# Kernel optimization log

Measured on AMD Instinct MI355X. Metric: run time of the kernel, lower is better.

## Reference

```python
import jax, jax.numpy as jnp
import numpy as np
import math

B, S, K, D, H, LH, W, L = 8, 2048, 128, 512, 8, 4, 128, 4
DH = D // H           # 64, head dim
NW = S // W           # 16 windows
NUM_STEPS = 1000
RESCALE = 4000.0


def setup_inputs() -> dict:
    key = jax.random.key(0)
    ks = iter(jax.random.split(key, 48))
    def rn(shape, s=0.02):
        return jax.random.normal(next(ks), shape, dtype=jnp.float32) * s
    return {
        "x": jax.random.normal(next(ks), (B, S, K), dtype=jnp.float32),
        "t": jax.random.randint(next(ks), (B,), 0, NUM_STEPS, dtype=jnp.int32),
        "token_w": rn((K, D)), "token_b": jnp.zeros((D,), jnp.float32),
        "ax1": rn((NW, D), 1.0), "ax2": rn((W, D), 1.0),
        "time_w1": rn((D, 4 * D)), "time_b1": jnp.zeros((4 * D,), jnp.float32),
        "time_w2": rn((4 * D, D)), "time_b2": jnp.zeros((D,), jnp.float32),
        "ln1_g": jnp.ones((L, D), jnp.float32), "ln1_b": jnp.zeros((L, D), jnp.float32),
        "wq": rn((L, D, D)), "wk": rn((L, D, D)), "wv": rn((L, D, D)),
        "wo": rn((L, D, D)), "wo_b": jnp.zeros((L, D), jnp.float32),
        "ln2_g": jnp.ones((L, D), jnp.float32), "ln2_b": jnp.zeros((L, D), jnp.float32),
        "ff_w1": rn((L, D, 4 * D)), "ff_b1": jnp.zeros((L, 4 * D), jnp.float32),
        "ff_w2": rn((L, 4 * D, D)), "ff_b2": jnp.zeros((L, D), jnp.float32),
        "norm_g": jnp.ones((D,), jnp.float32), "norm_b": jnp.zeros((D,), jnp.float32),
        "out_w": rn((D, K)), "out_b": jnp.zeros((K,), jnp.float32),
        "alpha": jax.random.normal(next(ks), (1,), dtype=jnp.float32),
    }


def _layernorm(x, g, b, eps=1e-5):
    mu = x.mean(-1, keepdims=True)
    var = ((x - mu) ** 2).mean(-1, keepdims=True)
    return (x - mu) * jax.lax.rsqrt(var + eps) * g + b


def _mish(x):
    return x * jnp.tanh(jax.nn.softplus(x))


def _sinusoidal(t):
    # SinusoidalPosEmb(dim=D, num_steps=NUM_STEPS, rescale_steps=4000)
    tt = t.astype(jnp.float32) / NUM_STEPS * RESCALE
    half = D // 2
    freqs = jnp.exp(jnp.arange(half, dtype=jnp.float32) * (-math.log(10000.0) / (half - 1)))
    e = tt[:, None] * freqs[None, :]
    return jnp.concatenate([jnp.sin(e), jnp.cos(e)], axis=-1)  # (B, D)


def _linear_attn(q, k, v):
    # non-causal kernelized linear attention; q,k,v: (B, h, S, dh)
    scale = DH ** -0.25
    q = jax.nn.softmax(q * scale, axis=-1)   # softmax over feature dim
    k = jax.nn.softmax(k * scale, axis=-2)   # softmax over sequence dim
    ctx = jnp.einsum('bhnd,bhne->bhde', k, v)
    return jnp.einsum('bhnd,bhde->bhne', q, ctx)


def _local_attn(q, k, v):
    # windowed softmax attention, window W, look_backward=1, look_forward=1
    b, h = q.shape[0], q.shape[1]
    qw = q.reshape(b, h, NW, W, DH) * (DH ** -0.5)
    def look_around(x):
        xw = x.reshape(b, h, NW, W, DH)
        xp = jnp.pad(xw, ((0, 0), (0, 0), (1, 1), (0, 0), (0, 0)))
        # keys of windows [i-1, i, i+1] -> (b, h, NW, 3W, dh)
        return jnp.concatenate([xp[:, :, :-2], xp[:, :, 1:-1], xp[:, :, 2:]], axis=3)
    kw, vw = look_around(k), look_around(v)
    win = jnp.arange(NW)[:, None] + (jnp.arange(3 * W) // W)[None, :] - 1  # (NW, 3W)
    valid = (win >= 0) & (win < NW)
    dots = jnp.einsum('bhnwd,bhnkd->bhnwk', qw, kw)
    mask_value = -jnp.finfo(dots.dtype).max
    dots = jnp.where(valid[None, None, :, None, :], dots, mask_value)
    attn = jax.nn.softmax(dots, axis=-1)
    out = jnp.einsum('bhnwk,bhnkd->bhnwd', attn, vw)
    return out.reshape(b, h, S, DH)


def reference(x, t, token_w, token_b, ax1, ax2, time_w1, time_b1, time_w2, time_b2,
              ln1_g, ln1_b, wq, wk, wv, wo, wo_b, ln2_g, ln2_b,
              ff_w1, ff_b1, ff_w2, ff_b2, norm_g, norm_b, out_w, out_b, alpha):
    te = _sinusoidal(t)
    te = _mish(te @ time_w1 + time_b1) @ time_w2 + time_b2          # (B, D)
    h = x @ token_w + token_b                                        # token embedding
    pos = (ax1[:, None, :] + ax2[None, :, :]).reshape(S, D)          # axial pos emb (summed)
    h = h + pos[None] + te[:, None, :]
    for l in range(L):
        n = _layernorm(h, ln1_g[l], ln1_b[l])
        def split_heads(y):
            return y.reshape(B, S, H, DH).transpose(0, 2, 1, 3)
        q = split_heads(n @ wq[l]); k = split_heads(n @ wk[l]); v = split_heads(n @ wv[l])
        lo = _local_attn(q[:, :LH], k[:, :LH], v[:, :LH])            # local heads first
        gl = _linear_attn(q[:, LH:], k[:, LH:], v[:, LH:])           # global linear-attn heads
        a = jnp.concatenate([lo, gl], axis=1).transpose(0, 2, 1, 3).reshape(B, S, D)
        h = h + a @ wo[l] + wo_b[l]
        n = _layernorm(h, ln2_g[l], ln2_b[l])
        h = h + jax.nn.gelu(n @ ff_w1[l] + ff_b1[l], approximate=False) @ ff_w2[l] + ff_b2[l]
    out = _layernorm(h, norm_g, norm_b) @ out_w + out_b              # (B, S, K)
    return alpha * out.transpose(0, 2, 1)                            # permute + Rezero -> (B, K, S)
```

## Files before the change

kernel.cpp:

```cpp
#include <hip/hip_runtime.h>

typedef __bf16 bf16;
typedef float f32x4 __attribute__((ext_vector_type(4)));
typedef __bf16 b8v __attribute__((ext_vector_type(8)));
typedef __bf16 b4v __attribute__((ext_vector_type(4)));

#define S_LEN 2048
#define DMODEL 512
#define KDIM 128
#define NWIN 16
#define WIN 128
#define QKVS 1536

__device__ inline f32x4 mfma16(b8v a, b8v b, f32x4 c) {
  return __builtin_amdgcn_mfma_f32_16x16x32_bf16(a, b, c, 0, 0, 0);
}

__device__ inline void gload16(const bf16* g, bf16* l) {
  __builtin_amdgcn_global_load_lds(
      (const __attribute__((address_space(1))) void*)g,
      (__attribute__((address_space(3))) void*)l, 16, 0, 0);
}

template<int N>
__device__ inline void waitvm() { asm volatile("s_waitcnt vmcnt(%0)" :: "n"(N) : "memory"); }
__device__ inline void barrier_raw() { asm volatile("s_barrier" ::: "memory"); }


__global__ __launch_bounds__(256) void conv_kernel(const float* __restrict__ in, bf16* __restrict__ out, int n) {
  int i4 = (blockIdx.x * 256 + threadIdx.x) * 4;
  if (i4 < n) {
    float4 v = *(const float4*)(in + i4);
    b4v o; o[0] = (bf16)v.x; o[1] = (bf16)v.y; o[2] = (bf16)v.z; o[3] = (bf16)v.w;
    *(b4v*)(out + i4) = o;
  }
}

__global__ __launch_bounds__(256) void convT_kernel(const float* __restrict__ W, bf16* __restrict__ WT,
                                                    int Kd, int N, size_t in_ls, size_t out_ls) {
  __shared__ float tile[32][33];
  int k0 = blockIdx.x * 32, n0 = blockIdx.y * 32;
  const float* Wl = W + (size_t)blockIdx.z * in_ls;
  bf16* WTl = WT + (size_t)blockIdx.z * out_ls;
  int tx = threadIdx.x & 31, ty = threadIdx.x >> 5;
  #pragma unroll
  for (int i = 0; i < 4; i++)
    tile[ty + i*8][tx] = Wl[(size_t)(k0 + ty + i*8) * N + n0 + tx];
  __syncthreads();
  #pragma unroll
  for (int i = 0; i < 4; i++)
    WTl[(size_t)(n0 + ty + i*8) * Kd + k0 + tx] = (bf16)tile[tx][ty + i*8];
}


__global__ __launch_bounds__(256) void time1_kernel(const int* __restrict__ t,
    const float* __restrict__ w1, const float* __restrict__ b1, float* __restrict__ te1) {
  __shared__ float te[512];
  __shared__ float red[4][64];
  int b = blockIdx.x >> 5;
  int c0 = (blockIdx.x & 31) * 64;
  int tid = threadIdx.x;
  float tt = (float)t[b] * 4.0f;
  {
    float fr = expf((float)tid * (-9.210340371976184f / 255.0f));
    float e = tt * fr;
    te[tid] = sinf(e);
    te[tid + 256] = cosf(e);
  }
  __syncthreads();
  int lane = tid & 63, wv = tid >> 6;
  float acc = 0.f;
  const float* wcol = w1 + (size_t)(wv * 128) * 2048 + c0 + lane;
  for (int dd = 0; dd < 128; dd++) acc = fmaf(te[wv * 128 + dd], wcol[(size_t)dd * 2048], acc);
  red[wv][lane] = acc;
  __syncthreads();
  if (tid < 64) {
    float a = red[0][tid] + red[1][tid] + red[2][tid] + red[3][tid] + b1[c0 + tid];
    float sp = (a > 20.f) ? a : log1pf(expf(a));
    te1[b * 2048 + c0 + tid] = a * tanhf(sp);
  }
}

__global__ __launch_bounds__(256) void time2_kernel(const float* __restrict__ te1,
    const float* __restrict__ w2, const float* __restrict__ b2, float* __restrict__ te2) {
  __shared__ float hb[2048];
  __shared__ float red[4][64];
  int b = blockIdx.x >> 3;
  int c0 = (blockIdx.x & 7) * 64;
  int tid = threadIdx.x;
  for (int i = tid; i < 2048; i += 256) hb[i] = te1[b * 2048 + i];
  __syncthreads();
  int lane = tid & 63, wv = tid >> 6;
  float acc = 0.f;
  const float* wcol = w2 + (size_t)(wv * 512) * 512 + c0 + lane;
  for (int dd = 0; dd < 512; dd++) acc = fmaf(hb[wv * 512 + dd], wcol[(size_t)dd * 512], acc);
  red[wv][lane] = acc;
  __syncthreads();
  if (tid < 64)
    te2[b * 512 + c0 + tid] = red[0][tid] + red[1][tid] + red[2][tid] + red[3][tid] + b2[c0 + tid];
}


__global__ __launch_bounds__(256) void ln_kernel(const float* __restrict__ hsrc,
    const float* __restrict__ gg, const float* __restrict__ bb, bf16* __restrict__ out) {
  int row = blockIdx.x * 4 + (threadIdx.x >> 6);
  int lane = threadIdx.x & 63;
  const float* hr = hsrc + (size_t)row * 512 + lane * 8;
  float4 v0 = *(const float4*)hr;
  float4 v1 = *(const float4*)(hr + 4);
  float xv[8] = {v0.x, v0.y, v0.z, v0.w, v1.x, v1.y, v1.z, v1.w};
  float s = 0.f;
  #pragma unroll
  for (int j = 0; j < 8; j++) s += xv[j];
  #pragma unroll
  for (int off = 1; off < 64; off <<= 1) s += __shfl_xor(s, off);
  float mu = s * (1.f / 512.f);
  float vs = 0.f;
  #pragma unroll
  for (int j = 0; j < 8; j++) { float dd = xv[j] - mu; vs += dd * dd; }
  #pragma unroll
  for (int off = 1; off < 64; off <<= 1) vs += __shfl_xor(vs, off);
  float rstd = 1.f / sqrtf(vs * (1.f / 512.f) + 1e-5f);
  int dbase = lane * 8;
  bf16* orow = out + (size_t)row * 512 + dbase;
  #pragma unroll
  for (int j = 0; j < 8; j++)
    orow[j] = (bf16)((xv[j] - mu) * rstd * gg[dbase + j] + bb[dbase + j]);
}

template<int EPI, int BM, int BN>
__global__ __launch_bounds__(512, 2) void gemm2_kernel(
    const bf16* __restrict__ A, const bf16* __restrict__ BT,
    const float* __restrict__ bias, float* __restrict__ Cf, bf16* __restrict__ Cb,
    int N, int Kd, int nbx) {
  constexpr int LA = BM / 128;
  constexpr int LB = BN / 128;
  constexpr int LPI = LA + LB;
  constexpr int EA = BM * 32;
  constexpr int EB = BN * 32;
  constexpr int ER = EA + EB;
  constexpr int MF = BM / 32;
  constexpr int NF = BN / 64;
  __shared__ bf16 lds[ER * 3];
  int tid = threadIdx.x;
  int lane = tid & 63, wid = tid >> 6;
  int g = lane >> 4, lr = lane & 15;
  int wm = wid >> 2, wn = wid & 3;
  int p = blockIdx.x;
  int cpx = (int)gridDim.x >> 3;
  int vid = (p & 7) * cpx + (p >> 3);
  int m0 = (vid / nbx) * BM;
  int n0 = (vid % nbx) * BN;
  f32x4 acc[MF][NF] = {};
  int rl = tid >> 2;
  int csw = ((tid & 3) ^ ((rl >> 1) & 3)) * 8;
  const bf16* pa = A + (size_t)(m0 + rl) * Kd + csw;
  const bf16* pb = BT + (size_t)(n0 + rl) * Kd + csw;
  int NT = Kd >> 5;
  auto stage = [&](int t, int buf) {
    int k0 = t << 5;
    bf16* base = lds + buf * ER + (wid << 9);
    #pragma unroll
    for (int rr = 0; rr < LA; rr++)
      gload16(pa + (size_t)(rr * 128) * Kd + k0, base + rr * 4096);
    #pragma unroll
    for (int rr = 0; rr < LB; rr++)
      gload16(pb + (size_t)(rr * 128) * Kd + k0, base + EA + rr * 4096);
  };
  stage(0, 0);
  stage(1, 1);
  waitvm<LPI>();
  barrier_raw();
  for (int t = 0; t < NT; ++t) {
    if (t + 2 < NT) stage(t + 2, (t + 2) % 3);
    const bf16* ba = lds + (t % 3) * ER;
    const bf16* bb = ba + EA;
    b8v af[MF], bfr[NF];
    #pragma unroll
    for (int i = 0; i < MF; i++) {
      int ra = wm * (BM / 2) + i * 16 + lr;
      af[i] = *(const b8v*)(ba + ra * 32 + ((g * 8) ^ (((ra >> 1) & 3) << 3)));
    }
    #pragma unroll
    for (int j = 0; j < NF; j++) {
      int rb = wn * (BN / 4) + j * 16 + lr;
      bfr[j] = *(const b8v*)(bb + rb * 32 + ((g * 8) ^ (((rb >> 1) & 3) << 3)));
    }
    __builtin_amdgcn_s_setprio(1);
    #pragma unroll
    for (int i = 0; i < MF; i++)
      #pragma unroll
      for (int j = 0; j < NF; j++)
        acc[i][j] = mfma16(af[i], bfr[j], acc[i][j]);
    __builtin_amdgcn_s_setprio(0);
    if (t + 1 < NT) {
      if (t + 2 < NT) waitvm<LPI>();
      else            waitvm<0>();
      barrier_raw();
    }
  }
  #pragma unroll
  for (int i = 0; i < MF; i++) {
    #pragma unroll
    for (int j = 0; j < NF; j++) {
      int col = n0 + wn * (BN / 4) + j * 16 + lr;
      float bv = (EPI != 0) ? bias[col] : 0.0f;
      #pragma unroll
      for (int r = 0; r < 4; r++) {
        int row = m0 + wm * (BM / 2) + i * 16 + g * 4 + r;
        float v = acc[i][j][r] + bv;
        if (EPI == 0) {
          Cb[(size_t)row * N + col] = (bf16)v;
        } else if (EPI == 2) {
          Cf[(size_t)row * N + col] += v;
        } else if (EPI == 3) {
          float ge = 0.5f * v * (1.0f + erff(v * 0.70710678118654752f));
          Cb[(size_t)row * N + col] = (bf16)ge;
        }
      }
    }
  }
}

template<int EPI>
__global__ __launch_bounds__(256) void gemm_kernel(
    const bf16* __restrict__ A, const bf16* __restrict__ BT,
    const float* __restrict__ bias, float* __restrict__ Cf, bf16* __restrict__ Cb,
    int N, int Kd, int nbx,
    const float* __restrict__ q1, const float* __restrict__ q2, const float* __restrict__ q3,
    const float* __restrict__ alphap) {
  __shared__ bf16 As[2][4096];
  __shared__ bf16 Bs[2][4096];
  int tid = threadIdx.x;
  int lane = tid & 63, wid = tid >> 6;
  int g = lane >> 4, lr = lane & 15;
  int wm = wid >> 1, wn = wid & 1;
  int p = blockIdx.x;
  int cpx = (int)gridDim.x >> 3;
  int vid = (p & 7) * cpx + (p >> 3);
  int m0 = (vid / nbx) * 128;
  int n0 = (vid % nbx) * 128;
  f32x4 acc[4][4] = {};
  int srow = wid * 16 + (lane >> 2);
  int scol = (lane & 3) * 8;
  const bf16* pa = A + (size_t)(m0 + srow) * Kd + scol;
  const bf16* pb = BT + (size_t)(n0 + srow) * Kd + scol;
  const size_t rstep = (size_t)64 * Kd;
  int nt = Kd >> 5;
  auto stage = [&](int buf, int k0) {
    bf16* lA = &As[buf][wid * 512];
    bf16* lB = &Bs[buf][wid * 512];
    gload16(pa + k0, lA);
    gload16(pa + rstep + k0, lA + 2048);
    gload16(pb + k0, lB);
    gload16(pb + rstep + k0, lB + 2048);
  };
  stage(0, 0);
  __syncthreads();
  int cur = 0;
  for (int t = 0; t < nt; ++t) {
    if (t + 1 < nt) stage(cur ^ 1, (t + 1) * 32);
    b8v af[4], bfv[4];
    #pragma unroll
    for (int i = 0; i < 4; i++) af[i]  = *(const b8v*)&As[cur][(wm * 64 + i * 16 + lr) * 32 + g * 8];
    #pragma unroll
    for (int i = 0; i < 4; i++) bfv[i] = *(const b8v*)&Bs[cur][(wn * 64 + i * 16 + lr) * 32 + g * 8];
    #pragma unroll
    for (int mf = 0; mf < 4; mf++)
      #pragma unroll
      for (int nf = 0; nf < 4; nf++)
        acc[mf][nf] = mfma16(af[mf], bfv[nf], acc[mf][nf]);
    __syncthreads();
    cur ^= 1;
  }
  if constexpr (EPI == 4) {
    __shared__ float Ts[32][130];
    float alp = alphap[0];
    int b_ = m0 >> 11, sb = m0 & 2047;
    #pragma unroll
    for (int cg = 0; cg < 4; cg++) {
      __syncthreads();
      if (wn == (cg >> 1)) {
        #pragma unroll
        for (int nfi = 0; nfi < 2; nfi++) {
          int nf = (cg & 1) * 2 + nfi;
          int cl = nfi * 16 + lr;
          float bv = bias[cg * 32 + cl];
          #pragma unroll
          for (int mf = 0; mf < 4; mf++)
            #pragma unroll
            for (int r = 0; r < 4; r++)
              Ts[cl][wm * 64 + mf * 16 + g * 4 + r] = alp * (acc[mf][nf][r] + bv);
        }
      }
      __syncthreads();
      int cl = tid >> 3, soff = (tid & 7) * 16;
      int col = cg * 32 + cl;
      float* dst = Cf + (size_t)b_ * (KDIM * S_LEN) + (size_t)col * S_LEN + sb + soff;
      #pragma unroll
      for (int q4 = 0; q4 < 4; q4++) {
        float4 v = {Ts[cl][soff + q4*4], Ts[cl][soff + q4*4 + 1], Ts[cl][soff + q4*4 + 2], Ts[cl][soff + q4*4 + 3]};
        *(float4*)(dst + q4 * 4) = v;
      }
    }
    return;
  }
  #pragma unroll
  for (int mf = 0; mf < 4; mf++) {
    #pragma unroll
    for (int nf = 0; nf < 4; nf++) {
      int col = n0 + wn * 64 + nf * 16 + lr;
      float bv = bias[col];
      #pragma unroll
      for (int r = 0; r < 4; r++) {
        int row = m0 + wm * 64 + mf * 16 + g * 4 + r;
        float v = acc[mf][nf][r] + bv;
        if (EPI == 5) {
          int b_ = row >> 11, s_ = row & 2047;
          float pv = q1[(s_ >> 7) * 512 + col] + q2[(s_ & 127) * 512 + col] + q3[b_ * 512 + col];
          Cf[(size_t)row * N + col] = v + pv;
        }
      }
    }
  }
}

__global__ __launch_bounds__(256) void locattn_kernel(
    const bf16* __restrict__ qkv, bf16* __restrict__ ab) {
  __shared__ bf16 Ks[128][72];
  __shared__ bf16 Vt[64][136];
  __shared__ bf16 Ps[4][32][136];
  int w = blockIdx.x;
  int b = blockIdx.y >> 2, hh = blockIdx.y & 3;
  int tid = threadIdx.x, wid = tid >> 6, lane = tid & 63;
  int g = lane >> 4, lr = lane & 15;
  const size_t rowb = (size_t)b * S_LEN * QKVS;
  int qrow0 = w * WIN + wid * 32;
  b8v qf[2][2];
  #pragma unroll
  for (int mf = 0; mf < 2; mf++)
    #pragma unroll
    for (int kf = 0; kf < 2; kf++)
      qf[mf][kf] = *(const b8v*)(qkv + rowb + (size_t)(qrow0 + mf * 16 + lr) * QKVS + hh * 64 + kf * 32 + g * 8);
  float mrun[2][4], lrun[2][4];
  f32x4 oacc[2][4] = {};
  #pragma unroll
  for (int mf = 0; mf < 2; mf++)
    #pragma unroll
    for (int r = 0; r < 4; r++) { mrun[mf][r] = -3e38f; lrun[mf][r] = 0.f; }
  for (int c = 0; c < 3; c++) {
    int wc = w - 1 + c;
    if (wc < 0 || wc >= NWIN) continue;
    __syncthreads();
    {
      int row = tid >> 1, f0 = (tid & 1) * 32;
      const bf16* kp = qkv + rowb + (size_t)(wc * WIN + row) * QKVS + 512 + hh * 64 + f0;
      #pragma unroll
      for (int i = 0; i < 4; i++)
        *(b8v*)&Ks[row][f0 + i * 8] = *(const b8v*)(kp + i * 8);
      const bf16* vp = qkv + rowb + (size_t)(wc * WIN + row) * QKVS + 1024 + hh * 64 + f0;
      #pragma unroll
      for (int i = 0; i < 4; i++) {
        b8v vv = *(const b8v*)(vp + i * 8);
        #pragma unroll
        for (int j = 0; j < 8; j++) Vt[f0 + i * 8 + j][row] = vv[j];
      }
    }
    __syncthreads();
    f32x4 sc[2][8] = {};
    #pragma unroll
    for (int nf = 0; nf < 8; nf++) {
      #pragma unroll
      for (int kf = 0; kf < 2; kf++) {
        b8v kfr = *(const b8v*)&Ks[nf * 16 + lr][kf * 32 + g * 8];
        sc[0][nf] = mfma16(qf[0][kf], kfr, sc[0][nf]);
        sc[1][nf] = mfma16(qf[1][kf], kfr, sc[1][nf]);
      }
    }
    #pragma unroll
    for (int mf = 0; mf < 2; mf++) {
      #pragma unroll
      for (int r = 0; r < 4; r++) {
        float cm = -3e38f;
        #pragma unroll
        for (int nf = 0; nf < 8; nf++) { sc[mf][nf][r] *= 0.125f; cm = fmaxf(cm, sc[mf][nf][r]); }
        cm = fmaxf(cm, __shfl_xor(cm, 1));
        cm = fmaxf(cm, __shfl_xor(cm, 2));
        cm = fmaxf(cm, __shfl_xor(cm, 4));
        cm = fmaxf(cm, __shfl_xor(cm, 8));
        float mnew = fmaxf(mrun[mf][r], cm);
        float corr = __expf(mrun[mf][r] - mnew);
        float rs = 0.f;
        #pragma unroll
        for (int nf = 0; nf < 8; nf++) { float p = __expf(sc[mf][nf][r] - mnew); sc[mf][nf][r] = p; rs += p; }
        rs += __shfl_xor(rs, 1); rs += __shfl_xor(rs, 2);
        rs += __shfl_xor(rs, 4); rs += __shfl_xor(rs, 8);
        lrun[mf][r] = lrun[mf][r] * corr + rs;
        mrun[mf][r] = mnew;
        #pragma unroll
        for (int vf = 0; vf < 4; vf++) oacc[mf][vf][r] *= corr;
      }
    }
    #pragma unroll
    for (int mf = 0; mf < 2; mf++)
      #pragma unroll
      for (int nf = 0; nf < 8; nf++)
        #pragma unroll
        for (int r = 0; r < 4; r++)
          Ps[wid][mf * 16 + g * 4 + r][nf * 16 + lr] = (bf16)sc[mf][nf][r];
    #pragma unroll
    for (int kf2 = 0; kf2 < 4; kf2++) {
      b8v pa0 = *(const b8v*)&Ps[wid][lr][kf2 * 32 + g * 8];
      b8v pa1 = *(const b8v*)&Ps[wid][16 + lr][kf2 * 32 + g * 8];
      #pragma unroll
      for (int vf = 0; vf < 4; vf++) {
        b8v vv = *(const b8v*)&Vt[vf * 16 + lr][kf2 * 32 + g * 8];
        oacc[0][vf] = mfma16(pa0, vv, oacc[0][vf]);
        oacc[1][vf] = mfma16(pa1, vv, oacc[1][vf]);
      }
    }
  }
  #pragma unroll
  for (int mf = 0; mf < 2; mf++) {
    #pragma unroll
    for (int r = 0; r < 4; r++) {
      float inv = 1.0f / lrun[mf][r];
      int row = qrow0 + mf * 16 + g * 4 + r;
      #pragma unroll
      for (int vf = 0; vf < 4; vf++)
        ab[(size_t)b * S_LEN * DMODEL + (size_t)row * DMODEL + hh * 64 + vf * 16 + lr] = (bf16)(oacc[mf][vf][r] * inv);
    }
  }
}


__global__ __launch_bounds__(256) void la2_kernel(const bf16* __restrict__ qkv,
    float* __restrict__ part, float* __restrict__ psum) {
  int ch = blockIdx.x, bh = blockIdx.y;
  int b = bh >> 2, hh = bh & 3;
  __shared__ float ke[128][65];
  __shared__ float vsh[128][65];
  __shared__ float red[4][64];
  int tid = threadIdx.x;
  const float scale = 0.35355339059327373f;
  const size_t base = ((size_t)b * S_LEN + (size_t)ch * 128) * QKVS;
  const bf16* kp = qkv + base + 768 + hh * 64;
  const bf16* vp = qkv + base + 1280 + hh * 64;
  for (int i = tid; i < 1024; i += 256) {
    int s = i >> 3, d0 = (i & 7) * 8;
    b8v kv = *(const b8v*)(kp + (size_t)s * QKVS + d0);
    b8v vv = *(const b8v*)(vp + (size_t)s * QKVS + d0);
    #pragma unroll
    for (int j = 0; j < 8; j++) {
      ke[s][d0 + j] = __expf((float)kv[j] * scale);
      vsh[s][d0 + j] = (float)vv[j];
    }
  }
  __syncthreads();
  int d = tid & 63, sg = tid >> 6;
  float ps = 0.f;
  for (int s = sg * 32; s < sg * 32 + 32; s++) ps += ke[s][d];
  red[sg][d] = ps;
  int e = tid & 63, dg = tid >> 6;
  float accv[16] = {};
  for (int s = 0; s < 128; s++) {
    float vv2 = vsh[s][e];
    #pragma unroll
    for (int i = 0; i < 16; i++) accv[i] = fmaf(ke[s][dg * 16 + i], vv2, accv[i]);
  }
  __syncthreads();
  float* pp = part + ((size_t)ch * 32 + bh) * 4096 + (size_t)dg * 16 * 64 + e;
  #pragma unroll
  for (int i = 0; i < 16; i++) pp[i * 64] = accv[i];
  if (tid < 64)
    psum[((size_t)ch * 32 + bh) * 64 + tid] = red[0][tid] + red[1][tid] + red[2][tid] + red[3][tid];
}

__global__ __launch_bounds__(256) void la2b_kernel(const float* __restrict__ part,
    const float* __restrict__ psum, float* __restrict__ ctx) {
  int idx = blockIdx.x * 256 + threadIdx.x;
  int bh = idx >> 12;
  int d = (idx >> 6) & 63;
  float s = 0.f, cs = 0.f;
  for (int c = 0; c < 16; c++) {
    s += part[(size_t)c * 131072 + idx];
    cs += psum[(size_t)(c * 32 + bh) * 64 + d];
  }
  ctx[idx] = s / cs;
}

__global__ __launch_bounds__(256) void la3_kernel(const bf16* __restrict__ qkv,
    const float* __restrict__ ctx, bf16* __restrict__ ab) {
  int ch = blockIdx.x, bh = blockIdx.y;
  int b = bh >> 2, hh = bh & 3;
  __shared__ float cs[64][65];
  int tid = threadIdx.x;
  for (int i = tid; i < 4096; i += 256) cs[i >> 6][i & 63] = ctx[(size_t)bh * 4096 + i];
  __syncthreads();
  int s = ch * 128 + (tid >> 1);
  int e0 = (tid & 1) * 32;
  const float scale = 0.35355339059327373f;
  const bf16* qr = qkv + ((size_t)b * S_LEN + s) * QKVS + 256 + hh * 64;
  float qv[64];
  float mx = -3e38f;
  #pragma unroll
  for (int i = 0; i < 8; i++) {
    b8v qq = *(const b8v*)(qr + i * 8);
    #pragma unroll
    for (int j = 0; j < 8; j++) { qv[i * 8 + j] = (float)qq[j] * scale; mx = fmaxf(mx, qv[i * 8 + j]); }
  }
  float sum = 0.f;
  #pragma unroll
  for (int dd = 0; dd < 64; dd++) { qv[dd] = __expf(qv[dd] - mx); sum += qv[dd]; }
  float inv = 1.f / sum;
  float o[32] = {};
  #pragma unroll
  for (int dd = 0; dd < 64; dd++) {
    float qq = qv[dd] * inv;
    #pragma unroll
    for (int j = 0; j < 32; j++) o[j] = fmaf(qq, cs[dd][e0 + j], o[j]);
  }
  bf16* op = ab + ((size_t)b * S_LEN + s) * DMODEL + 256 + hh * 64 + e0;
  #pragma unroll
  for (int j = 0; j < 32; j++) op[j] = (bf16)o[j];
}


extern "C" void kernel_launch(void* const* d_in, const int* in_sizes, int n_in,
                              void* d_out, int out_size, void* d_ws, size_t ws_size,
                              hipStream_t stream) {
  (void)in_sizes; (void)n_in; (void)out_size; (void)ws_size;
  const float* x_f     = (const float*)d_in[0];
  const int*   t_i     = (const int*)  d_in[1];
  const float* token_w = (const float*)d_in[2];
  const float* token_b = (const float*)d_in[3];
  const float* ax1     = (const float*)d_in[4];
  const float* ax2     = (const float*)d_in[5];
  const float* time_w1 = (const float*)d_in[6];
  const float* time_b1 = (const float*)d_in[7];
  const float* time_w2 = (const float*)d_in[8];
  const float* time_b2 = (const float*)d_in[9];
  const float* ln1_g   = (const float*)d_in[10];
  const float* ln1_b   = (const float*)d_in[11];
  const float* wq      = (const float*)d_in[12];
  const float* wk      = (const float*)d_in[13];
  const float* wv      = (const float*)d_in[14];
  const float* wo      = (const float*)d_in[15];
  const float* wo_b    = (const float*)d_in[16];
  const float* ln2_g   = (const float*)d_in[17];
  const float* ln2_b   = (const float*)d_in[18];
  const float* ff_w1   = (const float*)d_in[19];
  const float* ff_b1   = (const float*)d_in[20];
  const float* ff_w2   = (const float*)d_in[21];
  const float* ff_b2   = (const float*)d_in[22];
  const float* norm_g  = (const float*)d_in[23];
  const float* norm_b  = (const float*)d_in[24];
  const float* out_w   = (const float*)d_in[25];
  const float* out_b   = (const float*)d_in[26];
  const float* alpha   = (const float*)d_in[27];

  char* ws = (char*)d_ws;
  float* h      = (float*)(ws + 0);
  float* te1    = (float*)(ws + 33554432);
  float* te2    = (float*)(ws + 33619968);
  float* psum   = (float*)(ws + 33636352);
  float* ctx    = (float*)(ws + 33767424);
  float* part   = (float*)(ws + 34291712);
  bf16* nbuf    = (bf16*)(ws + 42680320);
  bf16* qkvb    = (bf16*)(ws + 59457536);
  bf16* abuf    = (bf16*)(ws + 109789184);
  bf16* gbuf    = qkvb;
  bf16* xw      = (bf16*)(ws + 126566400);
  bf16* token_wT= (bf16*)(ws + 130760704);
  bf16* wqkvT   = (bf16*)(ws + 130891776);
  bf16* woT     = (bf16*)(ws + 137183232);
  bf16* ff1T    = (bf16*)(ws + 139280384);
  bf16* ff2T    = (bf16*)(ws + 147668992);
  bf16* outwT   = (bf16*)(ws + 156057600);

  conv_kernel<<<2048, 256, 0, stream>>>(x_f, xw, 2097152);
  convT_kernel<<<dim3(4, 16, 1),  256, 0, stream>>>(token_w, token_wT, 128, 512, 65536, 65536);
  convT_kernel<<<dim3(16, 16, 4), 256, 0, stream>>>(wq, wqkvT,           512, 512, 262144, 786432);
  convT_kernel<<<dim3(16, 16, 4), 256, 0, stream>>>(wk, wqkvT + 262144,  512, 512, 262144, 786432);
  convT_kernel<<<dim3(16, 16, 4), 256, 0, stream>>>(wv, wqkvT + 524288,  512, 512, 262144, 786432);
  convT_kernel<<<dim3(16, 16, 4), 256, 0, stream>>>(wo, woT, 512, 512, 262144, 262144);
  convT_kernel<<<dim3(16, 64, 4), 256, 0, stream>>>(ff_w1, ff1T, 512, 2048, 1048576, 1048576);
  convT_kernel<<<dim3(64, 16, 4), 256, 0, stream>>>(ff_w2, ff2T, 2048, 512, 1048576, 1048576);
  convT_kernel<<<dim3(16, 4, 1),  256, 0, stream>>>(out_w, outwT, 512, 128, 65536, 65536);

  time1_kernel<<<256, 256, 0, stream>>>(t_i, time_w1, time_b1, te1);
  time2_kernel<<<64, 256, 0, stream>>>(te1, time_w2, time_b2, te2);

  gemm_kernel<5><<<512, 256, 0, stream>>>(xw, token_wT, token_b, h, nullptr, 512, 128, 4, ax1, ax2, te2, nullptr);

  for (int l = 0; l < 4; l++) {
    ln_kernel<<<4096, 256, 0, stream>>>(h, ln1_g + l * 512, ln1_b + l * 512, nbuf);
    gemm2_kernel<0, 128, 256><<<768, 512, 0, stream>>>(nbuf, wqkvT + (size_t)l * 786432, nullptr, nullptr, qkvb, 1536, 512, 6);
    locattn_kernel<<<dim3(16, 32), 256, 0, stream>>>(qkvb, abuf);
    la2_kernel<<<dim3(16, 32), 256, 0, stream>>>(qkvb, part, psum);
    la2b_kernel<<<512, 256, 0, stream>>>(part, psum, ctx);
    la3_kernel<<<dim3(16, 32), 256, 0, stream>>>(qkvb, ctx, abuf);
    gemm2_kernel<2, 128, 256><<<256, 512, 0, stream>>>(abuf, woT + (size_t)l * 262144, wo_b + l * 512, h, nullptr, 512, 512, 2);
    ln_kernel<<<4096, 256, 0, stream>>>(h, ln2_g + l * 512, ln2_b + l * 512, nbuf);
    gemm2_kernel<3, 256, 256><<<512, 512, 0, stream>>>(nbuf, ff1T + (size_t)l * 1048576, ff_b1 + l * 2048, nullptr, gbuf, 2048, 512, 8);
    gemm2_kernel<2, 128, 256><<<256, 512, 0, stream>>>(gbuf, ff2T + (size_t)l * 1048576, ff_b2 + l * 512, h, nullptr, 512, 2048, 2);
  }

  ln_kernel<<<4096, 256, 0, stream>>>(h, norm_g, norm_b, nbuf);
  gemm_kernel<4><<<128, 256, 0, stream>>>(nbuf, outwT, out_b, (float*)d_out, nullptr, 128, 512, 1, nullptr, nullptr, nullptr, alpha);
}
```

Baseline: 1.109 ms.

## Interleave B-fragment LDS loads with MFMAs and use tanh-approx GELU

Restructures the GEMM main loop so the wait and barrier come at the top of each k-step and the next prefetch is issued after the barrier. B fragments are then loaded from LDS one column-group ahead, with explicit lgkmcnt waits and sched barriers, so LDS reads overlap the MFMA issue. Separately, the exact erf-based GELU in the FF1 epilogue is replaced by the tanh approximation written as a sigmoid with __expf. That is cheaper but deviates from the reference's exact GELU.

```diff
diff --git a/kernel.cpp b/kernel.cpp
--- a/kernel.cpp
+++ b/kernel.cpp
@@ -24,6 +24,8 @@
 
 template<int N>
 __device__ inline void waitvm() { asm volatile("s_waitcnt vmcnt(%0)" :: "n"(N) : "memory"); }
+template<int N>
+__device__ inline void waitlgkm() { asm volatile("s_waitcnt lgkmcnt(%0)" :: "n"(N) : "memory"); }
 __device__ inline void barrier_raw() { asm volatile("s_barrier" ::: "memory"); }
 
 
@@ -129,7 +131,7 @@
 }
 
 template<int EPI, int BM, int BN>
-__global__ __launch_bounds__(512, 2) void gemm2_kernel(
+__global__ __launch_bounds__(512, 2) void gemm3_kernel(
     const bf16* __restrict__ A, const bf16* __restrict__ BT,
     const float* __restrict__ bias, float* __restrict__ Cf, bf16* __restrict__ Cb,
     int N, int Kd, int nbx) {
@@ -169,12 +171,13 @@
   };
   stage(0, 0);
   stage(1, 1);
-  waitvm<LPI>();
-  barrier_raw();
-  for (int t = 0; t < NT; ++t) {
-    if (t + 2 < NT) stage(t + 2, (t + 2) % 3);
-    const bf16* ba = lds + (t % 3) * ER;
+  for (int kt = 0; kt < NT; ++kt) {
+    if (kt + 1 < NT) waitvm<LPI>();
+    else             waitvm<0>();
+    barrier_raw();
+    const bf16* ba = lds + (kt % 3) * ER;
     const bf16* bb = ba + EA;
+    if (kt + 2 < NT) stage(kt + 2, (kt + 2) % 3);
     b8v af[MF], bfr[NF];
     #pragma unroll
     for (int i = 0; i < MF; i++) {
@@ -182,21 +185,30 @@
       af[i] = *(const b8v*)(ba + ra * 32 + ((g * 8) ^ (((ra >> 1) & 3) << 3)));
     }
     #pragma unroll
-    for (int j = 0; j < NF; j++) {
-      int rb = wn * (BN / 4) + j * 16 + lr;
-      bfr[j] = *(const b8v*)(bb + rb * 32 + ((g * 8) ^ (((rb >> 1) & 3) << 3)));
-    }
+    for (int j0 = 0; j0 < 2; j0++) {
+      int rb = wn * (BN / 4) + j0 * 16 + lr;
+      bfr[j0] = *(const b8v*)(bb + rb * 32 + ((g * 8) ^ (((rb >> 1) & 3) << 3)));
+    }
+    waitlgkm<0>();
+    __builtin_amdgcn_sched_barrier(0);
     __builtin_amdgcn_s_setprio(1);
     #pragma unroll
-    for (int i = 0; i < MF; i++)
-      #pragma unroll
-      for (int j = 0; j < NF; j++)
-        acc[i][j] = mfma16(af[i], bfr[j], acc[i][j]);
+    for (int i = 0; i < MF; i++) acc[i][0] = mfma16(af[i], bfr[0], acc[i][0]);
     __builtin_amdgcn_s_setprio(0);
-    if (t + 1 < NT) {
-      if (t + 2 < NT) waitvm<LPI>();
-      else            waitvm<0>();
-      barrier_raw();
+    #pragma unroll
+    for (int j = 1; j < NF; j++) {
+      if (j + 1 < NF) {
+        int rb = wn * (BN / 4) + (j + 1) * 16 + lr;
+        bfr[j + 1] = *(const b8v*)(bb + rb * 32 + ((g * 8) ^ (((rb >> 1) & 3) << 3)));
+        waitlgkm<1>();
+      } else {
+        waitlgkm<0>();
+      }
+      __builtin_amdgcn_sched_barrier(0);
+      __builtin_amdgcn_s_setprio(1);
+      #pragma unroll
+      for (int i = 0; i < MF; i++) acc[i][j] = mfma16(af[i], bfr[j], acc[i][j]);
+      __builtin_amdgcn_s_setprio(0);
     }
   }
   #pragma unroll
@@ -214,7 +226,8 @@
         } else if (EPI == 2) {
           Cf[(size_t)row * N + col] += v;
         } else if (EPI == 3) {
-          float ge = 0.5f * v * (1.0f + erff(v * 0.70710678118654752f));
+          float u = 1.5957691216057308f * (v + 0.044715f * v * v * v);
+          float ge = v / (1.0f + __expf(-u));
           Cb[(size_t)row * N + col] = (bf16)ge;
         }
       }
@@ -595,15 +608,15 @@
 
   for (int l = 0; l < 4; l++) {
     ln_kernel<<<4096, 256, 0, stream>>>(h, ln1_g + l * 512, ln1_b + l * 512, nbuf);
-    gemm2_kernel<0, 128, 256><<<768, 512, 0, stream>>>(nbuf, wqkvT + (size_t)l * 786432, nullptr, nullptr, qkvb, 1536, 512, 6);
+    gemm3_kernel<0, 128, 256><<<768, 512, 0, stream>>>(nbuf, wqkvT + (size_t)l * 786432, nullptr, nullptr, qkvb, 1536, 512, 6);
     locattn_kernel<<<dim3(16, 32), 256, 0, stream>>>(qkvb, abuf);
     la2_kernel<<<dim3(16, 32), 256, 0, stream>>>(qkvb, part, psum);
     la2b_kernel<<<512, 256, 0, stream>>>(part, psum, ctx);
     la3_kernel<<<dim3(16, 32), 256, 0, stream>>>(qkvb, ctx, abuf);
-    gemm2_kernel<2, 128, 256><<<256, 512, 0, stream>>>(abuf, woT + (size_t)l * 262144, wo_b + l * 512, h, nullptr, 512, 512, 2);
+    gemm3_kernel<2, 128, 256><<<256, 512, 0, stream>>>(abuf, woT + (size_t)l * 262144, wo_b + l * 512, h, nullptr, 512, 512, 2);
     ln_kernel<<<4096, 256, 0, stream>>>(h, ln2_g + l * 512, ln2_b + l * 512, nbuf);
-    gemm2_kernel<3, 256, 256><<<512, 512, 0, stream>>>(nbuf, ff1T + (size_t)l * 1048576, ff_b1 + l * 2048, nullptr, gbuf, 2048, 512, 8);
-    gemm2_kernel<2, 128, 256><<<256, 512, 0, stream>>>(gbuf, ff2T + (size_t)l * 1048576, ff_b2 + l * 512, h, nullptr, 512, 2048, 2);
+    gemm3_kernel<3, 256, 256><<<512, 512, 0, stream>>>(nbuf, ff1T + (size_t)l * 1048576, ff_b1 + l * 2048, nullptr, gbuf, 2048, 512, 8);
+    gemm3_kernel<2, 128, 256><<<256, 512, 0, stream>>>(gbuf, ff2T + (size_t)l * 1048576, ff_b2 + l * 512, h, nullptr, 512, 2048, 2);
   }
 
   ln_kernel<<<4096, 256, 0, stream>>>(h, norm_g, norm_b, nbuf);
```

After: 1.092 ms. About the same (-1.5%).

## Restructure GEMM to 256-row tiles with interleaved LDS loads and tanh GELU

Applied to the files above, without the earlier changes.

Replaces the GEMM kernel with a variant that always uses 256-row A tiles. For the QKV, WO and FF2 GEMMs the tile is now 256x128 instead of 128x256. The K-loop moves the wait/barrier to the top and issues the next stage after it, then splits the A-fragment LDS reads into phases interleaved with MFMA groups using sched_barrier. The FF1 epilogue swaps exact erf GELU for the tanh approximation written as a sigmoid with __expf. That approximation is cheaper but deviates from the reference's exact GELU.

```diff
diff --git a/kernel.cpp b/kernel.cpp
--- a/kernel.cpp
+++ b/kernel.cpp
@@ -128,18 +128,18 @@
     orow[j] = (bf16)((xv[j] - mu) * rstd * gg[dbase + j] + bb[dbase + j]);
 }
 
-template<int EPI, int BM, int BN>
-__global__ __launch_bounds__(512, 2) void gemm2_kernel(
+template<int EPI, int BN>
+__global__ __launch_bounds__(512, 2) void gemm4_kernel(
     const bf16* __restrict__ A, const bf16* __restrict__ BT,
     const float* __restrict__ bias, float* __restrict__ Cf, bf16* __restrict__ Cb,
     int N, int Kd, int nbx) {
-  constexpr int LA = BM / 128;
-  constexpr int LB = BN / 128;
+  constexpr int BM = 256;
+  constexpr int LA = 2, LB = BN / 128;
   constexpr int LPI = LA + LB;
   constexpr int EA = BM * 32;
   constexpr int EB = BN * 32;
   constexpr int ER = EA + EB;
-  constexpr int MF = BM / 32;
+  constexpr int MF = 8;
   constexpr int NF = BN / 64;
   __shared__ bf16 lds[ER * 3];
   int tid = threadIdx.x;
@@ -160,43 +160,51 @@
   auto stage = [&](int t, int buf) {
     int k0 = t << 5;
     bf16* base = lds + buf * ER + (wid << 9);
-    #pragma unroll
-    for (int rr = 0; rr < LA; rr++)
-      gload16(pa + (size_t)(rr * 128) * Kd + k0, base + rr * 4096);
+    gload16(pa + k0, base);
+    gload16(pa + (size_t)128 * Kd + k0, base + 4096);
     #pragma unroll
     for (int rr = 0; rr < LB; rr++)
       gload16(pb + (size_t)(rr * 128) * Kd + k0, base + EA + rr * 4096);
   };
+  auto ldA = [&](const bf16* ba, int f) -> b8v {
+    int ra = wm * 128 + f * 16 + lr;
+    return *(const b8v*)(ba + (ra & 127) * 32 + (ra >> 7) * 4096 +
+                         ((g * 8) ^ (((ra >> 1) & 3) << 3)));
+  };
   stage(0, 0);
   stage(1, 1);
-  waitvm<LPI>();
-  barrier_raw();
-  for (int t = 0; t < NT; ++t) {
-    if (t + 2 < NT) stage(t + 2, (t + 2) % 3);
-    const bf16* ba = lds + (t % 3) * ER;
+  for (int kt = 0; kt < NT; ++kt) {
+    if (kt + 1 < NT) waitvm<LPI>();
+    else             waitvm<0>();
+    barrier_raw();
+    const bf16* ba = lds + (kt % 3) * ER;
     const bf16* bb = ba + EA;
+    if (kt + 2 < NT) stage(kt + 2, (kt + 2) % 3);
     b8v af[MF], bfr[NF];
-    #pragma unroll
-    for (int i = 0; i < MF; i++) {
-      int ra = wm * (BM / 2) + i * 16 + lr;
-      af[i] = *(const b8v*)(ba + ra * 32 + ((g * 8) ^ (((ra >> 1) & 3) << 3)));
-    }
     #pragma unroll
     for (int j = 0; j < NF; j++) {
       int rb = wn * (BN / 4) + j * 16 + lr;
-      bfr[j] = *(const b8v*)(bb + rb * 32 + ((g * 8) ^ (((rb >> 1) & 3) << 3)));
-    }
-    __builtin_amdgcn_s_setprio(1);
-    #pragma unroll
-    for (int i = 0; i < MF; i++)
-      #pragma unroll
-      for (int j = 0; j < NF; j++)
-        acc[i][j] = mfma16(af[i], bfr[j], acc[i][j]);
-    __builtin_amdgcn_s_setprio(0);
-    if (t + 1 < NT) {
-      if (t + 2 < NT) waitvm<LPI>();
-      else            waitvm<0>();
-      barrier_raw();
+      bfr[j] = *(const b8v*)(bb + (rb & 127) * 32 + (rb >> 7) * 4096 +
+                             ((g * 8) ^ (((rb >> 1) & 3) << 3)));
+    }
+    af[0] = ldA(ba, 0);
+    af[1] = ldA(ba, 1);
+    __builtin_amdgcn_sched_barrier(0);
+    #pragma unroll
+    for (int ph = 0; ph < 4; ph++) {
+      if (ph < 3) {
+        af[2 * ph + 2] = ldA(ba, 2 * ph + 2);
+        af[2 * ph + 3] = ldA(ba, 2 * ph + 3);
+      }
+      __builtin_amdgcn_sched_barrier(0);
+      __builtin_amdgcn_s_setprio(1);
+      #pragma unroll
+      for (int i = 0; i < 2; i++)
+        #pragma unroll
+        for (int j = 0; j < NF; j++)
+          acc[2 * ph + i][j] = mfma16(af[2 * ph + i], bfr[j], acc[2 * ph + i][j]);
+      __builtin_amdgcn_s_setprio(0);
+      __builtin_amdgcn_sched_barrier(0);
     }
   }
   #pragma unroll
@@ -207,14 +215,15 @@
       float bv = (EPI != 0) ? bias[col] : 0.0f;
       #pragma unroll
       for (int r = 0; r < 4; r++) {
-        int row = m0 + wm * (BM / 2) + i * 16 + g * 4 + r;
+        int row = m0 + wm * 128 + i * 16 + g * 4 + r;
         float v = acc[i][j][r] + bv;
         if (EPI == 0) {
           Cb[(size_t)row * N + col] = (bf16)v;
         } else if (EPI == 2) {
           Cf[(size_t)row * N + col] += v;
         } else if (EPI == 3) {
-          float ge = 0.5f * v * (1.0f + erff(v * 0.70710678118654752f));
+          float u = 1.5957691216057308f * (v + 0.044715f * v * v * v);
+          float ge = v / (1.0f + __expf(-u));
           Cb[(size_t)row * N + col] = (bf16)ge;
         }
       }
@@ -595,15 +604,15 @@
 
   for (int l = 0; l < 4; l++) {
     ln_kernel<<<4096, 256, 0, stream>>>(h, ln1_g + l * 512, ln1_b + l * 512, nbuf);
-    gemm2_kernel<0, 128, 256><<<768, 512, 0, stream>>>(nbuf, wqkvT + (size_t)l * 786432, nullptr, nullptr, qkvb, 1536, 512, 6);
+    gemm4_kernel<0, 128><<<768, 512, 0, stream>>>(nbuf, wqkvT + (size_t)l * 786432, nullptr, nullptr, qkvb, 1536, 512, 12);
     locattn_kernel<<<dim3(16, 32), 256, 0, stream>>>(qkvb, abuf);
     la2_kernel<<<dim3(16, 32), 256, 0, stream>>>(qkvb, part, psum);
     la2b_kernel<<<512, 256, 0, stream>>>(part, psum, ctx);
     la3_kernel<<<dim3(16, 32), 256, 0, stream>>>(qkvb, ctx, abuf);
-    gemm2_kernel<2, 128, 256><<<256, 512, 0, stream>>>(abuf, woT + (size_t)l * 262144, wo_b + l * 512, h, nullptr, 512, 512, 2);
+    gemm4_kernel<2, 128><<<256, 512, 0, stream>>>(abuf, woT + (size_t)l * 262144, wo_b + l * 512, h, nullptr, 512, 512, 4);
     ln_kernel<<<4096, 256, 0, stream>>>(h, ln2_g + l * 512, ln2_b + l * 512, nbuf);
-    gemm2_kernel<3, 256, 256><<<512, 512, 0, stream>>>(nbuf, ff1T + (size_t)l * 1048576, ff_b1 + l * 2048, nullptr, gbuf, 2048, 512, 8);
-    gemm2_kernel<2, 128, 256><<<256, 512, 0, stream>>>(gbuf, ff2T + (size_t)l * 1048576, ff_b2 + l * 512, h, nullptr, 512, 2048, 2);
+    gemm4_kernel<3, 256><<<512, 512, 0, stream>>>(nbuf, ff1T + (size_t)l * 1048576, ff_b1 + l * 2048, nullptr, gbuf, 2048, 512, 8);
+    gemm4_kernel<2, 128><<<256, 512, 0, stream>>>(gbuf, ff2T + (size_t)l * 1048576, ff_b2 + l * 512, h, nullptr, 512, 2048, 4);
   }
 
   ln_kernel<<<4096, 256, 0, stream>>>(h, norm_g, norm_b, nbuf);
```

After: 1.098 ms. About the same (-1.0%).

## Replace 512-thread GEMM with 256-thread double-buffered kernel and tanh GELU

Applied to the files above, without the earlier changes.

Swaps the 512-thread, triple-buffered GEMM for a 256-thread kernel. It uses a fixed 128-row tile and a selectable column tile, double-buffered LDS, and a barrier before each compute step. The output projection and FF2 GEMMs now use 128-wide column tiles, doubling their grid, and FF1 uses a 1024-block grid. The exact erf GELU in the FF1 epilogue becomes the tanh approximation written as a sigmoid with __expf, which is cheaper but departs slightly from the reference's exact GELU. The shallower pipeline with an extra barrier per k-step may expose more memory latency than the previous three-stage scheme.

```diff
diff --git a/kernel.cpp b/kernel.cpp
--- a/kernel.cpp
+++ b/kernel.cpp
@@ -128,93 +128,84 @@
     orow[j] = (bf16)((xv[j] - mu) * rstd * gg[dbase + j] + bb[dbase + j]);
 }
 
-template<int EPI, int BM, int BN>
-__global__ __launch_bounds__(512, 2) void gemm2_kernel(
+template<int EPI, int BN>
+__global__ __launch_bounds__(256) void gemm6_kernel(
     const bf16* __restrict__ A, const bf16* __restrict__ BT,
     const float* __restrict__ bias, float* __restrict__ Cf, bf16* __restrict__ Cb,
     int N, int Kd, int nbx) {
-  constexpr int LA = BM / 128;
-  constexpr int LB = BN / 128;
-  constexpr int LPI = LA + LB;
-  constexpr int EA = BM * 32;
-  constexpr int EB = BN * 32;
-  constexpr int ER = EA + EB;
-  constexpr int MF = BM / 32;
-  constexpr int NF = BN / 64;
-  __shared__ bf16 lds[ER * 3];
-  int tid = threadIdx.x;
-  int lane = tid & 63, wid = tid >> 6;
+  constexpr int NF  = BN / 32;
+  constexpr int UB  = BN / 64;
+  constexpr int LPI = 2 + UB;
+  constexpr int AE  = 128 * 32;
+  constexpr int BE  = BN * 32;
+  constexpr int TE  = AE + BE;
+  __shared__ bf16 lds[TE * 2];
+  int tid = threadIdx.x, lane = tid & 63, wid = tid >> 6;
   int g = lane >> 4, lr = lane & 15;
-  int wm = wid >> 2, wn = wid & 3;
-  int p = blockIdx.x;
-  int cpx = (int)gridDim.x >> 3;
+  int wm = wid >> 1, wn = wid & 1;
+  int p = blockIdx.x, cpx = (int)gridDim.x >> 3;
   int vid = (p & 7) * cpx + (p >> 3);
-  int m0 = (vid / nbx) * BM;
-  int n0 = (vid % nbx) * BN;
-  f32x4 acc[MF][NF] = {};
+  int m0 = (vid / nbx) * 128, n0 = (vid % nbx) * BN;
+  f32x4 acc[4][NF] = {};
   int rl = tid >> 2;
   int csw = ((tid & 3) ^ ((rl >> 1) & 3)) * 8;
   const bf16* pa = A + (size_t)(m0 + rl) * Kd + csw;
   const bf16* pb = BT + (size_t)(n0 + rl) * Kd + csw;
   int NT = Kd >> 5;
-  auto stage = [&](int t, int buf) {
+  auto stage = [&](int t) {
     int k0 = t << 5;
-    bf16* base = lds + buf * ER + (wid << 9);
-    #pragma unroll
-    for (int rr = 0; rr < LA; rr++)
-      gload16(pa + (size_t)(rr * 128) * Kd + k0, base + rr * 4096);
-    #pragma unroll
-    for (int rr = 0; rr < LB; rr++)
-      gload16(pb + (size_t)(rr * 128) * Kd + k0, base + EA + rr * 4096);
+    bf16* base = lds + (t & 1) * TE + (wid << 9);
+    gload16(pa + k0, base);
+    gload16(pa + (size_t)64 * Kd + k0, base + 2048);
+    #pragma unroll
+    for (int u = 0; u < UB; u++)
+      gload16(pb + (size_t)(u * 64) * Kd + k0, base + AE + u * 2048);
   };
-  stage(0, 0);
-  stage(1, 1);
-  waitvm<LPI>();
-  barrier_raw();
+  stage(0);
   for (int t = 0; t < NT; ++t) {
-    if (t + 2 < NT) stage(t + 2, (t + 2) % 3);
-    const bf16* ba = lds + (t % 3) * ER;
-    const bf16* bb = ba + EA;
-    b8v af[MF], bfr[NF];
-    #pragma unroll
-    for (int i = 0; i < MF; i++) {
-      int ra = wm * (BM / 2) + i * 16 + lr;
+    bool more = (t + 1 < NT);
+    if (more) stage(t + 1);
+    if (more) waitvm<LPI>(); else waitvm<0>();
+    barrier_raw();
+    const bf16* ba = lds + (t & 1) * TE;
+    const bf16* bb = ba + AE;
+    b8v af[4], bfr[NF];
+    #pragma unroll
+    for (int i = 0; i < 4; i++) {
+      int ra = wm * 64 + i * 16 + lr;
       af[i] = *(const b8v*)(ba + ra * 32 + ((g * 8) ^ (((ra >> 1) & 3) << 3)));
     }
     #pragma unroll
     for (int j = 0; j < NF; j++) {
-      int rb = wn * (BN / 4) + j * 16 + lr;
+      int rb = wn * (BN / 2) + j * 16 + lr;
       bfr[j] = *(const b8v*)(bb + rb * 32 + ((g * 8) ^ (((rb >> 1) & 3) << 3)));
     }
     __builtin_amdgcn_s_setprio(1);
     #pragma unroll
-    for (int i = 0; i < MF; i++)
+    for (int i = 0; i < 4; i++)
       #pragma unroll
       for (int j = 0; j < NF; j++)
         acc[i][j] = mfma16(af[i], bfr[j], acc[i][j]);
     __builtin_amdgcn_s_setprio(0);
-    if (t + 1 < NT) {
-      if (t + 2 < NT) waitvm<LPI>();
-      else            waitvm<0>();
-      barrier_raw();
-    }
-  }
-  #pragma unroll
-  for (int i = 0; i < MF; i++) {
+    barrier_raw();
+  }
+  #pragma unroll
+  for (int i = 0; i < 4; i++) {
     #pragma unroll
     for (int j = 0; j < NF; j++) {
-      int col = n0 + wn * (BN / 4) + j * 16 + lr;
+      int col = n0 + wn * (BN / 2) + j * 16 + lr;
       float bv = (EPI != 0) ? bias[col] : 0.0f;
       #pragma unroll
       for (int r = 0; r < 4; r++) {
-        int row = m0 + wm * (BM / 2) + i * 16 + g * 4 + r;
+        int row = m0 + wm * 64 + i * 16 + g * 4 + r;
         float v = acc[i][j][r] + bv;
         if (EPI == 0) {
           Cb[(size_t)row * N + col] = (bf16)v;
         } else if (EPI == 2) {
           Cf[(size_t)row * N + col] += v;
         } else if (EPI == 3) {
-          float ge = 0.5f * v * (1.0f + erff(v * 0.70710678118654752f));
+          float u = 1.5957691216057308f * (v + 0.044715f * v * v * v);
+          float ge = v / (1.0f + __expf(-u));
           Cb[(size_t)row * N + col] = (bf16)ge;
         }
       }
@@ -595,15 +586,15 @@
 
   for (int l = 0; l < 4; l++) {
     ln_kernel<<<4096, 256, 0, stream>>>(h, ln1_g + l * 512, ln1_b + l * 512, nbuf);
-    gemm2_kernel<0, 128, 256><<<768, 512, 0, stream>>>(nbuf, wqkvT + (size_t)l * 786432, nullptr, nullptr, qkvb, 1536, 512, 6);
+    gemm6_kernel<0, 256><<<768, 256, 0, stream>>>(nbuf, wqkvT + (size_t)l * 786432, nullptr, nullptr, qkvb, 1536, 512, 6);
     locattn_kernel<<<dim3(16, 32), 256, 0, stream>>>(qkvb, abuf);
     la2_kernel<<<dim3(16, 32), 256, 0, stream>>>(qkvb, part, psum);
     la2b_kernel<<<512, 256, 0, stream>>>(part, psum, ctx);
     la3_kernel<<<dim3(16, 32), 256, 0, stream>>>(qkvb, ctx, abuf);
-    gemm2_kernel<2, 128, 256><<<256, 512, 0, stream>>>(abuf, woT + (size_t)l * 262144, wo_b + l * 512, h, nullptr, 512, 512, 2);
+    gemm6_kernel<2, 128><<<512, 256, 0, stream>>>(abuf, woT + (size_t)l * 262144, wo_b + l * 512, h, nullptr, 512, 512, 4);
     ln_kernel<<<4096, 256, 0, stream>>>(h, ln2_g + l * 512, ln2_b + l * 512, nbuf);
-    gemm2_kernel<3, 256, 256><<<512, 512, 0, stream>>>(nbuf, ff1T + (size_t)l * 1048576, ff_b1 + l * 2048, nullptr, gbuf, 2048, 512, 8);
-    gemm2_kernel<2, 128, 256><<<256, 512, 0, stream>>>(gbuf, ff2T + (size_t)l * 1048576, ff_b2 + l * 512, h, nullptr, 512, 2048, 2);
+    gemm6_kernel<3, 256><<<1024, 256, 0, stream>>>(nbuf, ff1T + (size_t)l * 1048576, ff_b1 + l * 2048, nullptr, gbuf, 2048, 512, 8);
+    gemm6_kernel<2, 128><<<512, 256, 0, stream>>>(gbuf, ff2T + (size_t)l * 1048576, ff_b2 + l * 512, h, nullptr, 512, 2048, 4);
   }
 
   ln_kernel<<<4096, 256, 0, stream>>>(h, norm_g, norm_b, nbuf);
```

Result: slower. 1.229 ms (+10.8%).
